# Kernel tuning notes

Hardware: AMD Instinct MI355X
Metric: run time of the kernel (lower is better)

Reference implementation:

```python
import jax, jax.numpy as jnp
import numpy as np

B, H, W, C = 1, 64, 512, 256
NH, HS, WS = 8, 4, 32
T = HS * WS            # tokens per window = 128
HD = C // NH           # head dim = 32
L = H * W
SCALE = HD ** -0.5
HID = 4 * C            # mlp hidden
EPS = 1e-5


def _ln(x, g, b):
    m = jnp.mean(x, axis=-1, keepdims=True)
    v = jnp.var(x, axis=-1, keepdims=True)
    return (x - m) * jax.lax.rsqrt(v + EPS) * g + b


def setup_inputs() -> dict:
    key = jax.random.key(0)
    ks = jax.random.split(key, 16)
    def rn(k, shape, s=0.02):
        return jax.random.normal(k, shape, jnp.float32) * s
    return {
        "x": jax.random.normal(ks[0], (B, L, C), jnp.float32),
        "pos": jax.random.normal(ks[1], (B, L, 2), jnp.float32),
        "norm1_g": jnp.ones((C,), jnp.float32), "norm1_b": jnp.zeros((C,), jnp.float32),
        "wq": rn(ks[2], (C, C)), "bq": jnp.zeros((C,), jnp.float32),
        "wk": rn(ks[3], (C, C)), "bk": jnp.zeros((C,), jnp.float32),
        "wv": rn(ks[4], (C, C)), "bv": jnp.zeros((C,), jnp.float32),
        "wo": rn(ks[5], (C, C)), "bo": jnp.zeros((C,), jnp.float32),
        "norm2_g": jnp.ones((C,), jnp.float32), "norm2_b": jnp.zeros((C,), jnp.float32),
        "w_fc1": rn(ks[6], (C, HID)), "b_fc1": jnp.zeros((HID,), jnp.float32),
        "w_fc2": rn(ks[7], (HID, C)), "b_fc2": jnp.zeros((C,), jnp.float32),
        # pos_embedding_cart: Conv1d(2->16,k1), BN1d(16) (inference), ReLU, Conv1d(16->NH,k1)
        "pw1": rn(ks[8], (16, 2), 0.1), "pb1": jnp.zeros((16,), jnp.float32),
        "bn_g": jnp.ones((16,), jnp.float32), "bn_b": jnp.zeros((16,), jnp.float32),
        "bn_m": jnp.zeros((16,), jnp.float32), "bn_v": jnp.ones((16,), jnp.float32),
        "pw2": rn(ks[9], (NH, 16), 0.1), "pb2": jnp.zeros((NH,), jnp.float32),
    }


def _to_windows(t):  # [B,L,C] -> [nW, T, C]
    t = t.reshape(B, H // HS, HS, W // WS, WS, C).transpose(0, 1, 3, 2, 4, 5)
    return t.reshape(-1, T, C)


def _to_heads(t):  # [B,L,C] -> [nW, NH, T, HD]
    return _to_windows(t).reshape(-1, T, NH, HD).transpose(0, 2, 1, 3)


def reference(x, pos, norm1_g, norm1_b, wq, bq, wk, bk, wv, bv, wo, bo,
              norm2_g, norm2_b, w_fc1, b_fc1, w_fc2, b_fc2,
              pw1, pb1, bn_g, bn_b, bn_m, bn_v, pw2, pb2):
    shortcut = x
    xn = _ln(x, norm1_g, norm1_b)

    # relative position bias per window via 1x1 conv net (BN in inference mode)
    posw = pos.reshape(B, H // HS, HS, W // WS, WS, 2).transpose(0, 1, 3, 5, 2, 4)
    posw = posw.reshape(-1, 2, T)                               # [nW, 2, T]
    rel = posw[:, :, :, None] - posw[:, :, None, :]             # [nW, 2, T, T]
    h = jnp.einsum('oc,nctu->notu', pw1, rel) + pb1[None, :, None, None]
    h = (h - bn_m[None, :, None, None]) * jax.lax.rsqrt(bn_v + EPS)[None, :, None, None]
    h = h * bn_g[None, :, None, None] + bn_b[None, :, None, None]
    h = jax.nn.relu(h)
    bias = jnp.einsum('oc,nctu->notu', pw2, h) + pb2[None, :, None, None]  # [nW, NH, T, T]

    q = _to_heads(xn @ wq + bq) * SCALE
    k = _to_heads(xn @ wk + bk)
    v = _to_heads(xn @ wv + bv)

    attn = jax.nn.softmax(jnp.einsum('nhtd,nhud->nhtu', q, k) + bias, axis=-1)
    o = jnp.einsum('nhtu,nhud->nhtd', attn, v)                  # [nW, NH, T, HD]
    o = o.transpose(0, 2, 1, 3).reshape(-1, T, C)               # [nW, T, C]
    o = o.reshape(B, H // HS, W // WS, HS, WS, C).transpose(0, 1, 3, 2, 4, 5)
    o = o.reshape(B, L, C) @ wo + bo

    x1 = shortcut + o
    mlp = jax.nn.gelu(_ln(x1, norm2_g, norm2_b) @ w_fc1 + b_fc1, approximate=False) @ w_fc2 + b_fc2
    return x1 + mlp
```

## Files before the change

### kernel.cpp

```cpp
#include <hip/hip_runtime.h>
#include <cstdint>

typedef unsigned short u16;
typedef __bf16 bf16x8 __attribute__((ext_vector_type(8)));
typedef float f32x4 __attribute__((ext_vector_type(4)));

#define LN_EPS 1e-5f
#define SCALE_Q 0.17677669529663689f

__device__ __forceinline__ u16 f2bf(float f) {
    union { float f; unsigned int i; } c; c.f = f;
    unsigned int r = c.i + 0x7FFFu + ((c.i >> 16) & 1u);
    return (u16)(r >> 16);
}
__device__ __forceinline__ unsigned pack2(float hi, float lo) {
    return __builtin_amdgcn_perm(__float_as_uint(hi), __float_as_uint(lo), 0x07060302u);
}
__device__ __forceinline__ void async16(const void* g, void* l) {
    __builtin_amdgcn_global_load_lds(
        (__attribute__((address_space(1))) unsigned int*)(unsigned long long)g,
        (__attribute__((address_space(3))) unsigned int*)l, 16, 0, 0);
}

__global__ void transpose_all(const float* __restrict__ wq, const float* __restrict__ wk,
                              const float* __restrict__ wv, const float* __restrict__ wo,
                              const float* __restrict__ f1, const float* __restrict__ f2,
                              u16* oq, u16* ok, u16* ov, u16* oo, u16* o1, u16* o2) {
    __shared__ float tile[32][33];
    const int b = blockIdx.x;
    const float* In; u16* Out; int R, C, bx, by;
    if (b < 256) {
        const int m = b >> 6, l = b & 63;
        In = m == 0 ? wq : (m == 1 ? wk : (m == 2 ? wv : wo));
        Out = m == 0 ? oq : (m == 1 ? ok : (m == 2 ? ov : oo));
        R = 256; C = 256; bx = (l & 7) * 32; by = (l >> 3) * 32;
    } else if (b < 512) {
        const int l = b - 256; In = f1; Out = o1; R = 256; C = 1024;
        bx = (l & 31) * 32; by = (l >> 5) * 32;
    } else {
        const int l = b - 512; In = f2; Out = o2; R = 1024; C = 256;
        bx = (l & 7) * 32; by = (l >> 3) * 32;
    }
    const int tx = threadIdx.x, ty = threadIdx.y;
    for (int i = 0; i < 32; i += 8)
        tile[ty + i][tx] = In[(size_t)(by + ty + i) * C + bx + tx];
    __syncthreads();
    for (int i = 0; i < 32; i += 8)
        Out[(size_t)(bx + ty + i) * R + by + tx] = f2bf(tile[tx][ty + i]);
}

__global__ __launch_bounds__(256) void ln_k(const float* __restrict__ X, const float* __restrict__ G,
                                            const float* __restrict__ Bt, u16* __restrict__ Y) {
    const int token = blockIdx.x * 4 + (threadIdx.x >> 6);
    const int ln = threadIdx.x & 63;
    const float4 rv = *(const float4*)(X + (size_t)token * 256 + ln * 4);
    float s = rv.x + rv.y + rv.z + rv.w;
    float q = rv.x * rv.x + rv.y * rv.y + rv.z * rv.z + rv.w * rv.w;
    #pragma unroll
    for (int m = 1; m < 64; m <<= 1) { s += __shfl_xor(s, m, 64); q += __shfl_xor(q, m, 64); }
    const float mean = s * (1.f / 256.f);
    const float var  = q * (1.f / 256.f) - mean * mean;
    const float rs   = rsqrtf(var + LN_EPS);
    const float4 gv = *(const float4*)(G + ln * 4);
    const float4 bv = *(const float4*)(Bt + ln * 4);
    ushort4 o;
    o.x = f2bf((rv.x - mean) * rs * gv.x + bv.x);
    o.y = f2bf((rv.y - mean) * rs * gv.y + bv.y);
    o.z = f2bf((rv.z - mean) * rs * gv.z + bv.z);
    o.w = f2bf((rv.w - mean) * rs * gv.w + bv.w);
    *(ushort4*)(Y + (size_t)token * 256 + ln * 4) = o;
}

__global__ __launch_bounds__(256, 2) void gemm_bt(
    const u16* __restrict__ X, const u16* __restrict__ Wt,
    const float* __restrict__ B1, const float* __restrict__ B2, const float* __restrict__ B3,
    const float* __restrict__ Res,
    u16* __restrict__ Ybf, float* __restrict__ Yf,
    int M, int N, int K, int mode) {
    __shared__ alignas(16) u16 sBuf[128 * 128];
    u16* sA = sBuf;
    u16* sB = sBuf + 128 * 64;
    const int tid = threadIdx.x, wv = tid >> 6, ln = tid & 63;
    const int quad = ln >> 4, l16 = ln & 15;
    const int m0 = blockIdx.y * 128, n0 = blockIdx.x * 128;
    const int mw = (wv >> 1) * 64, nw = (wv & 1) * 64;
    const int r8 = ln >> 3, c8 = ln & 7;
    const f32x4 z4 = {0.f, 0.f, 0.f, 0.f};
    f32x4 acc[4][4];
    #pragma unroll
    for (int i = 0; i < 4; i++)
        #pragma unroll
        for (int j = 0; j < 4; j++) acc[i][j] = z4;

    for (int k0 = 0; k0 < K; k0 += 64) {
        __syncthreads();
        #pragma unroll
        for (int i = 0; i < 4; i++) {
            const int row = wv * 32 + i * 8;
            async16(X  + (size_t)(m0 + row + r8) * K + k0 + c8 * 8, &sA[row * 64]);
            async16(Wt + (size_t)(n0 + row + r8) * K + k0 + c8 * 8, &sB[row * 64]);
        }
        __syncthreads();
        #pragma unroll
        for (int kk = 0; kk < 2; kk++) {
            bf16x8 af[4], bfr[4];
            #pragma unroll
            for (int i = 0; i < 4; i++) af[i]  = *(const bf16x8*)&sA[(mw + i * 16 + l16) * 64 + kk * 32 + quad * 8];
            #pragma unroll
            for (int j = 0; j < 4; j++) bfr[j] = *(const bf16x8*)&sB[(nw + j * 16 + l16) * 64 + kk * 32 + quad * 8];
            #pragma unroll
            for (int i = 0; i < 4; i++)
                #pragma unroll
                for (int j = 0; j < 4; j++)
                    acc[i][j] = __builtin_amdgcn_mfma_f32_16x16x32_bf16(af[i], bfr[j], acc[i][j], 0, 0, 0);
        }
    }
    const int seg = n0 >> 8;
    const float* bp = (mode == 4) ? (seg == 0 ? B1 : (seg == 1 ? B2 : B3)) : B1;
    const float sc = (mode == 4 && seg == 0) ? SCALE_Q : 1.f;
    if (mode == 4) {
        __syncthreads();
        #pragma unroll
        for (int j = 0; j < 4; j++) {
            const int col = nw + j * 16 + l16;
            const float bc = bp[(n0 + col) & 255];
            #pragma unroll
            for (int i = 0; i < 4; i++)
                #pragma unroll
                for (int r = 0; r < 4; r++)
                    sBuf[(mw + i * 16 + quad * 4 + r) * 128 + col] = f2bf((acc[i][j][r] + bc) * sc);
        }
        __syncthreads();
        #pragma unroll
        for (int it = 0; it < 8; it++) {
            const int idx = it * 256 + tid;
            const int row = idx >> 4, sg = idx & 15;
            *(uint4*)(Ybf + (size_t)(m0 + row) * N + n0 + sg * 8) = *(const uint4*)&sBuf[row * 128 + sg * 8];
        }
    } else {
        #pragma unroll
        for (int j = 0; j < 4; j++) {
            const int col = n0 + nw + j * 16 + l16;
            const float bc = bp[col];
            #pragma unroll
            for (int i = 0; i < 4; i++) {
                #pragma unroll
                for (int r = 0; r < 4; r++) {
                    const int row = m0 + mw + i * 16 + quad * 4 + r;
                    float v = acc[i][j][r] + bc;
                    if (mode == 2) v += Res[(size_t)row * N + col];
                    Yf[(size_t)row * N + col] = v;
                }
            }
        }
    }
}

__global__ __launch_bounds__(256) void bias_k(
    const float* __restrict__ pos, const float* __restrict__ pw1, const float* __restrict__ pb1,
    const float* __restrict__ bng, const float* __restrict__ bnb, const float* __restrict__ bnm,
    const float* __restrict__ bnv, const float* __restrict__ pw2, u16* __restrict__ Bg) {
    __shared__ float sTa[32 * 128], sTa2[32 * 128];
    __shared__ u16 sW[16 * 32];
    __shared__ alignas(16) u16 sOut[4][8 * 128];
    const int n = blockIdx.x, wh = n >> 4, ww = n & 15;
    const int tid = threadIdx.x, wv = tid >> 6, ln = tid & 63;
    const int quad = ln >> 4, l16 = ln & 15;
    for (int r = 0; r < 16; r++) {
        const int e = tid + r * 256, o = e >> 7, t = e & 127;
        float ta = 0.f, ta2 = 0.f;
        if (o < 16) {
            const int l = (wh * 4 + (t >> 5)) * 512 + ww * 32 + (t & 31);
            const float sv = rsqrtf(bnv[o] + LN_EPS) * bng[o];
            ta = sv * (pw1[o * 2] * pos[l * 2] + pw1[o * 2 + 1] * pos[l * 2 + 1]);
            ta2 = ta + (pb1[o] - bnm[o]) * sv + bnb[o];
        }
        sTa[o * 128 + t] = ta; sTa2[o * 128 + t] = ta2;
    }
    for (int r = 0; r < 2; r++) {
        const int e = tid + r * 256, h = e >> 5, o = e & 31;
        sW[e] = (h < 8 && o < 16) ? f2bf(pw2[h * 16 + o]) : (u16)0;
    }
    __syncthreads();
    const bf16x8 af = *(const bf16x8*)&sW[l16 * 32 + quad * 8];
    float uo[8][8];
    #pragma unroll
    for (int c = 0; c < 8; c++)
        #pragma unroll
        for (int j = 0; j < 8; j++)
            uo[c][j] = sTa[(quad * 8 + j) * 128 + c * 16 + l16];
    const f32x4 z4 = {0.f, 0.f, 0.f, 0.f};
    u16* outb = Bg + (size_t)n * 131072;
    for (int tl = 0; tl < 32; tl++) {
        const int t = wv * 32 + tl;
        float t2[8];
        #pragma unroll
        for (int j = 0; j < 8; j++) t2[j] = sTa2[(quad * 8 + j) * 128 + t];
        #pragma unroll
        for (int c = 0; c < 8; c++) {
            float rl[8];
            #pragma unroll
            for (int j = 0; j < 8; j++) rl[j] = fmaxf(t2[j] - uo[c][j], 0.f);
            union { unsigned u[4]; bf16x8 v; } bb;
            #pragma unroll
            for (int p = 0; p < 4; p++) bb.u[p] = pack2(rl[2 * p + 1], rl[2 * p]);
            const f32x4 cc = __builtin_amdgcn_mfma_f32_16x16x32_bf16(af, bb.v, z4, 0, 0, 0);
            if (quad < 2) {
                #pragma unroll
                for (int r = 0; r < 4; r++)
                    sOut[wv][(quad * 4 + r) * 128 + c * 16 + l16] =
                        (u16)(__float_as_uint(cc[r]) >> 16);
            }
        }
        #pragma unroll
        for (int it = 0; it < 2; it++) {
            const int idx = it * 64 + ln;
            const int h = idx >> 4, u8 = idx & 15;
            *(uint4*)(outb + (size_t)h * 16384 + t * 128 + u8 * 8) = *(const uint4*)&sOut[wv][idx * 8];
        }
    }
}

__global__ __launch_bounds__(256, 2) void attn_k(
    const u16* __restrict__ Qkv, const u16* __restrict__ Bg, u16* __restrict__ Ob) {
    constexpr int SPS = 136;
    __shared__ alignas(16) u16 sQ[128 * 32];
    __shared__ alignas(16) u16 sK[128 * 32];
    __shared__ alignas(16) u16 sVt[32 * 128];
    __shared__ alignas(16) u16 sPB[128 * SPS];

    const int n = blockIdx.x, h = blockIdx.y;
    const int tid = threadIdx.x, wv = tid >> 6, ln = tid & 63;
    const int quad = ln >> 4, l16 = ln & 15;
    const int wh = n >> 4, ww = n & 15;

    {
        const int tb = wv * 16 + (ln >> 2);
        const int d8 = ln & 3;
        #pragma unroll
        for (int i = 0; i < 2; i++) {
            const int tt = tb + i * 64;
            const int l = (wh * 4 + (tt >> 5)) * 512 + ww * 32 + (tt & 31);
            const size_t g = (size_t)l * 768 + h * 32 + d8 * 8;
            async16(Qkv + g, &sQ[(wv * 16 + i * 64) * 32]);
            async16(Qkv + g + 256, &sK[(wv * 16 + i * 64) * 32]);
        }
        const u16* bsrc = Bg + (size_t)(n * 8 + h) * 16384;
        #pragma unroll
        for (int rr = 0; rr < 8; rr++)
            async16(bsrc + rr * 2048 + wv * 512 + ln * 8, &sPB[rr * 2048 + wv * 512]);
        #pragma unroll
        for (int i = 0; i < 2; i++) {
            const int tt = tb + i * 64;
            const int l = (wh * 4 + (tt >> 5)) * 512 + ww * 32 + (tt & 31);
            const uint4 raw = *(const uint4*)(Qkv + (size_t)l * 768 + 512 + h * 32 + d8 * 8);
            const u16* e = (const u16*)&raw;
            #pragma unroll
            for (int j = 0; j < 8; j++) sVt[(d8 * 8 + j) * 128 + tt] = e[j];
        }
    }
    __syncthreads();

    const f32x4 z4 = {0.f, 0.f, 0.f, 0.f};
    f32x4 acc[2][8];
    {
        bf16x8 qf[2], kf[8];
        #pragma unroll
        for (int i = 0; i < 2; i++) qf[i] = *(const bf16x8*)&sQ[(wv * 32 + i * 16 + l16) * 32 + quad * 8];
        #pragma unroll
        for (int j = 0; j < 8; j++) kf[j] = *(const bf16x8*)&sK[(j * 16 + l16) * 32 + quad * 8];
        #pragma unroll
        for (int i = 0; i < 2; i++)
            #pragma unroll
            for (int j = 0; j < 8; j++)
                acc[i][j] = __builtin_amdgcn_mfma_f32_16x16x32_bf16(qf[i], kf[j], z4, 0, 0, 0);
    }
    #pragma unroll
    for (int i = 0; i < 2; i++)
        #pragma unroll
        for (int j = 0; j < 8; j++)
            #pragma unroll
            for (int r = 0; r < 4; r++) {
                const int t = wv * 32 + i * 16 + quad * 4 + r;
                const unsigned bu = sPB[t * 128 + j * 16 + l16];
                acc[i][j][r] += __uint_as_float(bu << 16);
            }
    float rinv[2][4];
    #pragma unroll
    for (int i = 0; i < 2; i++) {
        #pragma unroll
        for (int r = 0; r < 4; r++) {
            float mx = acc[i][0][r];
            #pragma unroll
            for (int j = 1; j < 8; j++) mx = fmaxf(mx, acc[i][j][r]);
            #pragma unroll
            for (int m = 1; m < 16; m <<= 1) mx = fmaxf(mx, __shfl_xor(mx, m, 64));
            float sm = 0.f;
            #pragma unroll
            for (int j = 0; j < 8; j++) {
                const float p = __expf(acc[i][j][r] - mx);
                acc[i][j][r] = p;
                sm += p;
            }
            #pragma unroll
            for (int m = 1; m < 16; m <<= 1) sm += __shfl_xor(sm, m, 64);
            rinv[i][r] = 1.f / sm;
        }
    }
    __syncthreads();
    #pragma unroll
    for (int i = 0; i < 2; i++)
        #pragma unroll
        for (int j = 0; j < 8; j++)
            #pragma unroll
            for (int r = 0; r < 4; r++) {
                const int t = wv * 32 + i * 16 + quad * 4 + r;
                sPB[t * SPS + j * 16 + l16] = (u16)(__float_as_uint(acc[i][j][r]) >> 16);
            }
    __syncthreads();
    f32x4 oacc[2][2];
    #pragma unroll
    for (int i = 0; i < 2; i++)
        #pragma unroll
        for (int jd = 0; jd < 2; jd++) oacc[i][jd] = z4;
    #pragma unroll
    for (int ku = 0; ku < 4; ku++) {
        bf16x8 pf[2], vf[2];
        #pragma unroll
        for (int i = 0; i < 2; i++) pf[i] = *(const bf16x8*)&sPB[(wv * 32 + i * 16 + l16) * SPS + ku * 32 + quad * 8];
        #pragma unroll
        for (int jd = 0; jd < 2; jd++) vf[jd] = *(const bf16x8*)&sVt[(jd * 16 + l16) * 128 + ku * 32 + quad * 8];
        #pragma unroll
        for (int i = 0; i < 2; i++)
            #pragma unroll
            for (int jd = 0; jd < 2; jd++)
                oacc[i][jd] = __builtin_amdgcn_mfma_f32_16x16x32_bf16(pf[i], vf[jd], oacc[i][jd], 0, 0, 0);
    }
    #pragma unroll
    for (int i = 0; i < 2; i++)
        #pragma unroll
        for (int jd = 0; jd < 2; jd++)
            #pragma unroll
            for (int r = 0; r < 4; r++) {
                const int t = wv * 32 + i * 16 + quad * 4 + r;
                const int d = jd * 16 + l16;
                const int l = (wh * 4 + (t >> 5)) * 512 + ww * 32 + (t & 31);
                Ob[(size_t)l * 256 + h * 32 + d] = f2bf(oacc[i][jd][r] * rinv[i][r]);
            }
}

__global__ __launch_bounds__(256, 2) void mlp_fused(
    const u16* __restrict__ Xn, const u16* __restrict__ fc1T, const u16* __restrict__ fc2T,
    const float* __restrict__ b1, const float* __restrict__ b2, float* __restrict__ Out) {
    __shared__ alignas(16) u16 sA[64 * 256];
    __shared__ alignas(16) u16 sW[128 * 128];
    __shared__ alignas(16) u16 sH[64 * 128];
    const int tid = threadIdx.x, wv = tid >> 6, ln = tid & 63;
    const int quad = ln >> 4, l16 = ln & 15;
    const int m0 = blockIdx.x * 64;
    const int mw = (wv >> 1) * 32;
    const int nw1 = (wv & 1) * 64;
    const int nw2 = (wv & 1) * 128;

    #pragma unroll
    for (int rr = 0; rr < 8; rr++) {
        const int row2 = rr * 8 + wv * 2;
        const int row = row2 + (ln >> 5);
        const int kb = (ln & 31) ^ (row & 7);
        async16(Xn + (size_t)(m0 + row) * 256 + kb * 8, &sA[row2 * 256]);
    }

    const f32x4 z4 = {0.f, 0.f, 0.f, 0.f};
    f32x4 acc2[2][8];
    #pragma unroll
    for (int i = 0; i < 2; i++)
        #pragma unroll
        for (int j = 0; j < 8; j++) acc2[i][j] = z4;

    for (int c = 0; c < 8; c++) {
        f32x4 acc1[2][4];
        #pragma unroll
        for (int i = 0; i < 2; i++)
            #pragma unroll
            for (int j = 0; j < 4; j++) acc1[i][j] = z4;
        #pragma unroll
        for (int kc0 = 0; kc0 < 2; kc0++) {
            __syncthreads();
            #pragma unroll
            for (int rr = 0; rr < 8; rr++) {
                const int r4 = wv * 32 + rr * 4;
                const int row = r4 + (ln >> 4);
                const int kb = (ln & 15) ^ (row & 15);
                async16(fc1T + (size_t)(c * 128 + row) * 256 + kc0 * 128 + kb * 8, &sW[r4 * 128]);
            }
            __syncthreads();
            #pragma unroll
            for (int kk = 0; kk < 4; kk++) {
                bf16x8 af[2], bfr[4];
                #pragma unroll
                for (int i = 0; i < 2; i++) {
                    const int ra = mw + i * 16 + l16;
                    const int b = kc0 * 16 + kk * 4 + quad;
                    af[i] = *(const bf16x8*)&sA[ra * 256 + ((b ^ (ra & 7)) * 8)];
                }
                #pragma unroll
                for (int j = 0; j < 4; j++) {
                    const int rb = nw1 + j * 16 + l16;
                    const int b = kk * 4 + quad;
                    bfr[j] = *(const bf16x8*)&sW[rb * 128 + ((b ^ (rb & 15)) * 8)];
                }
                #pragma unroll
                for (int i = 0; i < 2; i++)
                    #pragma unroll
                    for (int j = 0; j < 4; j++)
                        acc1[i][j] = __builtin_amdgcn_mfma_f32_16x16x32_bf16(af[i], bfr[j], acc1[i][j], 0, 0, 0);
            }
        }
        #pragma unroll
        for (int j = 0; j < 4; j++) {
            const float bc = b1[c * 128 + nw1 + j * 16 + l16];
            const int col = nw1 + j * 16 + l16;
            const int blk = col >> 3, off = col & 7;
            #pragma unroll
            for (int i = 0; i < 2; i++)
                #pragma unroll
                for (int r = 0; r < 4; r++) {
                    float v = acc1[i][j][r] + bc;
                    const float p = v * v;
                    const float qq = fmaf(p, -0.07135481283f, -1.5957691216f);
                    v = v / (1.f + __expf(v * qq));
                    const int row = mw + i * 16 + quad * 4 + r;
                    sH[row * 128 + ((blk ^ (row & 15)) * 8) + off] = f2bf(v);
                }
        }
        #pragma unroll
        for (int kc0 = 0; kc0 < 2; kc0++) {
            __syncthreads();
            #pragma unroll
            for (int rr = 0; rr < 8; rr++) {
                const int r8 = wv * 64 + rr * 8;
                const int row = r8 + (ln >> 3);
                const int kb = (ln & 7) ^ (row & 7);
                async16(fc2T + (size_t)row * 1024 + c * 128 + kc0 * 64 + kb * 8, &sW[r8 * 64]);
            }
            __syncthreads();
            #pragma unroll
            for (int kk = 0; kk < 2; kk++) {
                bf16x8 pf[2], bfr[8];
                #pragma unroll
                for (int i = 0; i < 2; i++) {
                    const int rp = mw + i * 16 + l16;
                    const int b = kc0 * 8 + kk * 4 + quad;
                    pf[i] = *(const bf16x8*)&sH[rp * 128 + ((b ^ (rp & 15)) * 8)];
                }
                #pragma unroll
                for (int j = 0; j < 8; j++) {
                    const int rb = nw2 + j * 16 + l16;
                    const int b = kk * 4 + quad;
                    bfr[j] = *(const bf16x8*)&sW[rb * 64 + ((b ^ (rb & 7)) * 8)];
                }
                #pragma unroll
                for (int i = 0; i < 2; i++)
                    #pragma unroll
                    for (int j = 0; j < 8; j++)
                        acc2[i][j] = __builtin_amdgcn_mfma_f32_16x16x32_bf16(pf[i], bfr[j], acc2[i][j], 0, 0, 0);
            }
        }
    }
    #pragma unroll
    for (int j = 0; j < 8; j++) {
        const int col = nw2 + j * 16 + l16;
        const float bc = b2[col];
        #pragma unroll
        for (int i = 0; i < 2; i++)
            #pragma unroll
            for (int r = 0; r < 4; r++) {
                const size_t idx = (size_t)(m0 + mw + i * 16 + quad * 4 + r) * 256 + col;
                Out[idx] = acc2[i][j][r] + bc + Out[idx];
            }
    }
}

extern "C" void kernel_launch(void* const* d_in, const int* in_sizes, int n_in,
                              void* d_out, int out_size, void* d_ws, size_t ws_size,
                              hipStream_t stream) {
    const float* x    = (const float*)d_in[0];
    const float* pos  = (const float*)d_in[1];
    const float* n1g  = (const float*)d_in[2];
    const float* n1b  = (const float*)d_in[3];
    const float* wq   = (const float*)d_in[4];
    const float* bq   = (const float*)d_in[5];
    const float* wk   = (const float*)d_in[6];
    const float* bk   = (const float*)d_in[7];
    const float* wvw  = (const float*)d_in[8];
    const float* bv   = (const float*)d_in[9];
    const float* wo   = (const float*)d_in[10];
    const float* bo   = (const float*)d_in[11];
    const float* n2g  = (const float*)d_in[12];
    const float* n2b  = (const float*)d_in[13];
    const float* wfc1 = (const float*)d_in[14];
    const float* bfc1 = (const float*)d_in[15];
    const float* wfc2 = (const float*)d_in[16];
    const float* bfc2 = (const float*)d_in[17];
    const float* pw1  = (const float*)d_in[18];
    const float* pb1  = (const float*)d_in[19];
    const float* bng  = (const float*)d_in[20];
    const float* bnb  = (const float*)d_in[21];
    const float* bnm  = (const float*)d_in[22];
    const float* bnv  = (const float*)d_in[23];
    const float* pw2  = (const float*)d_in[24];
    float* out = (float*)d_out;
    u16* ws  = (u16*)d_ws;

    const size_t SZ = (size_t)32768 * 256;
    u16* s0   = ws;
    u16* qkv  = ws + SZ;
    u16* wqT  = ws + 4 * SZ;
    u16* wkT  = wqT + 65536;
    u16* wvT  = wkT + 65536;
    u16* woT  = wvT + 65536;
    u16* fc1T = woT + 65536;
    u16* fc2T = fc1T + 262144;
    u16* biasg = fc2T + 262144;

    transpose_all<<<768, dim3(32, 8), 0, stream>>>(wq, wk, wvw, wo, wfc1, wfc2,
                                                   wqT, wkT, wvT, woT, fc1T, fc2T);
    ln_k<<<8192, 256, 0, stream>>>(x, n1g, n1b, s0);
    gemm_bt<<<dim3(6, 256), 256, 0, stream>>>(s0, wqT, bq, bk, bv, nullptr, qkv, nullptr,
                                              32768, 768, 256, 4);
    bias_k<<<256, 256, 0, stream>>>(pos, pw1, pb1, bng, bnb, bnm, bnv, pw2, biasg);
    attn_k<<<dim3(256, 8), 256, 0, stream>>>(qkv, biasg, s0);
    gemm_bt<<<dim3(2, 256), 256, 0, stream>>>(s0, woT, bo, nullptr, nullptr, x, nullptr, out,
                                              32768, 256, 256, 2);
    ln_k<<<8192, 256, 0, stream>>>(out, n2g, n2b, s0);
    mlp_fused<<<512, 256, 0, stream>>>(s0, fc1T, fc2T, bfc1, bfc2, out);
}
```

Before: 322.4 us.

## Swizzle LDS layouts in gemm/attn and double-buffer fused MLP weight staging

Applies XOR swizzles to the LDS tiles in the generic GEMM (A and B) and in the attention kernel (Q, K and transposed V), so that MFMA fragment reads and V scatter writes avoid bank conflicts. In the fused MLP kernel, the single 128x128 weight buffer is split into two 64x128 ping-pong buffers with smaller k-chunks. The next fc1/fc2 chunk, and the first fc1 chunk of the following column block, now prefetch while the current chunk is computed. This removes one barrier per stage and hides global load latency, in exchange for more chunks and more complex index arithmetic.

```diff
diff --git a/kernel.cpp b/kernel.cpp
--- a/kernel.cpp
+++ b/kernel.cpp
@@ -84,7 +84,8 @@
     const int quad = ln >> 4, l16 = ln & 15;
     const int m0 = blockIdx.y * 128, n0 = blockIdx.x * 128;
     const int mw = (wv >> 1) * 64, nw = (wv & 1) * 64;
-    const int r8 = ln >> 3, c8 = ln & 7;
+    const int r8 = ln >> 3;
+    const int kbs = (ln & 7) ^ (r8 & 7);
     const f32x4 z4 = {0.f, 0.f, 0.f, 0.f};
     f32x4 acc[4][4];
     #pragma unroll
@@ -97,17 +98,25 @@
         #pragma unroll
         for (int i = 0; i < 4; i++) {
             const int row = wv * 32 + i * 8;
-            async16(X  + (size_t)(m0 + row + r8) * K + k0 + c8 * 8, &sA[row * 64]);
-            async16(Wt + (size_t)(n0 + row + r8) * K + k0 + c8 * 8, &sB[row * 64]);
+            async16(X  + (size_t)(m0 + row + r8) * K + k0 + kbs * 8, &sA[row * 64]);
+            async16(Wt + (size_t)(n0 + row + r8) * K + k0 + kbs * 8, &sB[row * 64]);
         }
         __syncthreads();
         #pragma unroll
         for (int kk = 0; kk < 2; kk++) {
             bf16x8 af[4], bfr[4];
             #pragma unroll
-            for (int i = 0; i < 4; i++) af[i]  = *(const bf16x8*)&sA[(mw + i * 16 + l16) * 64 + kk * 32 + quad * 8];
-            #pragma unroll
-            for (int j = 0; j < 4; j++) bfr[j] = *(const bf16x8*)&sB[(nw + j * 16 + l16) * 64 + kk * 32 + quad * 8];
+            for (int i = 0; i < 4; i++) {
+                const int ra = mw + i * 16 + l16;
+                const int b = kk * 4 + quad;
+                af[i] = *(const bf16x8*)&sA[ra * 64 + ((b ^ (ra & 7)) * 8)];
+            }
+            #pragma unroll
+            for (int j = 0; j < 4; j++) {
+                const int rb = nw + j * 16 + l16;
+                const int b = kk * 4 + quad;
+                bfr[j] = *(const bf16x8*)&sB[rb * 64 + ((b ^ (rb & 7)) * 8)];
+            }
             #pragma unroll
             for (int i = 0; i < 4; i++)
                 #pragma unroll
@@ -235,13 +244,14 @@
     const int wh = n >> 4, ww = n & 15;
 
     {
-        const int tb = wv * 16 + (ln >> 2);
-        const int d8 = ln & 3;
+        const int rw = ln >> 2;
+        const int tb = wv * 16 + rw;
+        const int kbq = (ln & 3) ^ (rw & 3);
         #pragma unroll
         for (int i = 0; i < 2; i++) {
             const int tt = tb + i * 64;
             const int l = (wh * 4 + (tt >> 5)) * 512 + ww * 32 + (tt & 31);
-            const size_t g = (size_t)l * 768 + h * 32 + d8 * 8;
+            const size_t g = (size_t)l * 768 + h * 32 + kbq * 8;
             async16(Qkv + g, &sQ[(wv * 16 + i * 64) * 32]);
             async16(Qkv + g + 256, &sK[(wv * 16 + i * 64) * 32]);
         }
@@ -249,6 +259,7 @@
         #pragma unroll
         for (int rr = 0; rr < 8; rr++)
             async16(bsrc + rr * 2048 + wv * 512 + ln * 8, &sPB[rr * 2048 + wv * 512]);
+        const int d8 = ln & 3;
         #pragma unroll
         for (int i = 0; i < 2; i++) {
             const int tt = tb + i * 64;
@@ -256,7 +267,10 @@
             const uint4 raw = *(const uint4*)(Qkv + (size_t)l * 768 + 512 + h * 32 + d8 * 8);
             const u16* e = (const u16*)&raw;
             #pragma unroll
-            for (int j = 0; j < 8; j++) sVt[(d8 * 8 + j) * 128 + tt] = e[j];
+            for (int j = 0; j < 8; j++) {
+                const int row = d8 * 8 + j;
+                sVt[row * 128 + (((tt >> 3) ^ (row & 15)) * 8) + (tt & 7)] = e[j];
+            }
         }
     }
     __syncthreads();
@@ -266,9 +280,15 @@
     {
         bf16x8 qf[2], kf[8];
         #pragma unroll
-        for (int i = 0; i < 2; i++) qf[i] = *(const bf16x8*)&sQ[(wv * 32 + i * 16 + l16) * 32 + quad * 8];
-        #pragma unroll
-        for (int j = 0; j < 8; j++) kf[j] = *(const bf16x8*)&sK[(j * 16 + l16) * 32 + quad * 8];
+        for (int i = 0; i < 2; i++) {
+            const int t = wv * 32 + i * 16 + l16;
+            qf[i] = *(const bf16x8*)&sQ[t * 32 + ((quad ^ (t & 3)) * 8)];
+        }
+        #pragma unroll
+        for (int j = 0; j < 8; j++) {
+            const int t = j * 16 + l16;
+            kf[j] = *(const bf16x8*)&sK[t * 32 + ((quad ^ (t & 3)) * 8)];
+        }
         #pragma unroll
         for (int i = 0; i < 2; i++)
             #pragma unroll
@@ -329,7 +349,11 @@
         #pragma unroll
         for (int i = 0; i < 2; i++) pf[i] = *(const bf16x8*)&sPB[(wv * 32 + i * 16 + l16) * SPS + ku * 32 + quad * 8];
         #pragma unroll
-        for (int jd = 0; jd < 2; jd++) vf[jd] = *(const bf16x8*)&sVt[(jd * 16 + l16) * 128 + ku * 32 + quad * 8];
+        for (int jd = 0; jd < 2; jd++) {
+            const int rv = jd * 16 + l16;
+            const int b = ku * 4 + quad;
+            vf[jd] = *(const bf16x8*)&sVt[rv * 128 + ((b ^ (rv & 15)) * 8)];
+        }
         #pragma unroll
         for (int i = 0; i < 2; i++)
             #pragma unroll
@@ -353,7 +377,8 @@
     const u16* __restrict__ Xn, const u16* __restrict__ fc1T, const u16* __restrict__ fc2T,
     const float* __restrict__ b1, const float* __restrict__ b2, float* __restrict__ Out) {
     __shared__ alignas(16) u16 sA[64 * 256];
-    __shared__ alignas(16) u16 sW[128 * 128];
+    __shared__ alignas(16) u16 sW0[64 * 128];
+    __shared__ alignas(16) u16 sW1[64 * 128];
     __shared__ alignas(16) u16 sH[64 * 128];
     const int tid = threadIdx.x, wv = tid >> 6, ln = tid & 63;
     const int quad = ln >> 4, l16 = ln & 15;
@@ -362,6 +387,25 @@
     const int nw1 = (wv & 1) * 64;
     const int nw2 = (wv & 1) * 128;
 
+    auto stage_f1 = [&](int c, int kc, u16* buf) {
+        #pragma unroll
+        for (int rr = 0; rr < 4; rr++) {
+            const int r0 = (rr * 4 + wv) * 8;
+            const int row = r0 + (ln >> 3);
+            const int kb = (ln & 7) ^ (row & 7);
+            async16(fc1T + (size_t)(c * 128 + row) * 256 + kc * 64 + kb * 8, &buf[r0 * 64]);
+        }
+    };
+    auto stage_f2 = [&](int c, int kc, u16* buf) {
+        #pragma unroll
+        for (int rr = 0; rr < 4; rr++) {
+            const int r0 = (rr * 4 + wv) * 16;
+            const int row = r0 + (ln >> 2);
+            const int kb = (ln & 3) ^ (row & 3);
+            async16(fc2T + (size_t)row * 1024 + c * 128 + kc * 32 + kb * 8, &buf[r0 * 32]);
+        }
+    };
+
     #pragma unroll
     for (int rr = 0; rr < 8; rr++) {
         const int row2 = rr * 8 + wv * 2;
@@ -369,6 +413,7 @@
         const int kb = (ln & 31) ^ (row & 7);
         async16(Xn + (size_t)(m0 + row) * 256 + kb * 8, &sA[row2 * 256]);
     }
+    stage_f1(0, 0, sW0);
 
     const f32x4 z4 = {0.f, 0.f, 0.f, 0.f};
     f32x4 acc2[2][8];
@@ -377,6 +422,7 @@
         #pragma unroll
         for (int j = 0; j < 8; j++) acc2[i][j] = z4;
 
+    __syncthreads();
     for (int c = 0; c < 8; c++) {
         f32x4 acc1[2][4];
         #pragma unroll
@@ -384,30 +430,24 @@
             #pragma unroll
             for (int j = 0; j < 4; j++) acc1[i][j] = z4;
         #pragma unroll
-        for (int kc0 = 0; kc0 < 2; kc0++) {
-            __syncthreads();
-            #pragma unroll
-            for (int rr = 0; rr < 8; rr++) {
-                const int r4 = wv * 32 + rr * 4;
-                const int row = r4 + (ln >> 4);
-                const int kb = (ln & 15) ^ (row & 15);
-                async16(fc1T + (size_t)(c * 128 + row) * 256 + kc0 * 128 + kb * 8, &sW[r4 * 128]);
-            }
-            __syncthreads();
-            #pragma unroll
-            for (int kk = 0; kk < 4; kk++) {
+        for (int kc = 0; kc < 4; kc++) {
+            u16* cur = (kc & 1) ? sW1 : sW0;
+            u16* nxt = (kc & 1) ? sW0 : sW1;
+            if (kc < 3) stage_f1(c, kc + 1, nxt);
+            #pragma unroll
+            for (int kk = 0; kk < 2; kk++) {
                 bf16x8 af[2], bfr[4];
                 #pragma unroll
                 for (int i = 0; i < 2; i++) {
                     const int ra = mw + i * 16 + l16;
-                    const int b = kc0 * 16 + kk * 4 + quad;
+                    const int b = kc * 8 + kk * 4 + quad;
                     af[i] = *(const bf16x8*)&sA[ra * 256 + ((b ^ (ra & 7)) * 8)];
                 }
                 #pragma unroll
                 for (int j = 0; j < 4; j++) {
                     const int rb = nw1 + j * 16 + l16;
                     const int b = kk * 4 + quad;
-                    bfr[j] = *(const bf16x8*)&sW[rb * 128 + ((b ^ (rb & 15)) * 8)];
+                    bfr[j] = *(const bf16x8*)&cur[rb * 64 + ((b ^ (rb & 7)) * 8)];
                 }
                 #pragma unroll
                 for (int i = 0; i < 2; i++)
@@ -415,7 +455,9 @@
                     for (int j = 0; j < 4; j++)
                         acc1[i][j] = __builtin_amdgcn_mfma_f32_16x16x32_bf16(af[i], bfr[j], acc1[i][j], 0, 0, 0);
             }
-        }
+            __syncthreads();
+        }
+        stage_f2(c, 0, sW0);
         #pragma unroll
         for (int j = 0; j < 4; j++) {
             const float bc = b1[c * 128 + nw1 + j * 16 + l16];
@@ -433,38 +475,31 @@
                     sH[row * 128 + ((blk ^ (row & 15)) * 8) + off] = f2bf(v);
                 }
         }
-        #pragma unroll
-        for (int kc0 = 0; kc0 < 2; kc0++) {
+        __syncthreads();
+        #pragma unroll
+        for (int kc = 0; kc < 4; kc++) {
+            u16* cur = (kc & 1) ? sW1 : sW0;
+            u16* nxt = (kc & 1) ? sW0 : sW1;
+            if (kc < 3) stage_f2(c, kc + 1, nxt);
+            else if (c < 7) stage_f1(c + 1, 0, nxt);
+            bf16x8 pf[2], bfr[8];
+            #pragma unroll
+            for (int i = 0; i < 2; i++) {
+                const int rp = mw + i * 16 + l16;
+                const int b = kc * 4 + quad;
+                pf[i] = *(const bf16x8*)&sH[rp * 128 + ((b ^ (rp & 15)) * 8)];
+            }
+            #pragma unroll
+            for (int j = 0; j < 8; j++) {
+                const int rb = nw2 + j * 16 + l16;
+                bfr[j] = *(const bf16x8*)&cur[rb * 32 + ((quad ^ (rb & 3)) * 8)];
+            }
+            #pragma unroll
+            for (int i = 0; i < 2; i++)
+                #pragma unroll
+                for (int j = 0; j < 8; j++)
+                    acc2[i][j] = __builtin_amdgcn_mfma_f32_16x16x32_bf16(pf[i], bfr[j], acc2[i][j], 0, 0, 0);
             __syncthreads();
-            #pragma unroll
-            for (int rr = 0; rr < 8; rr++) {
-                const int r8 = wv * 64 + rr * 8;
-                const int row = r8 + (ln >> 3);
-                const int kb = (ln & 7) ^ (row & 7);
-                async16(fc2T + (size_t)row * 1024 + c * 128 + kc0 * 64 + kb * 8, &sW[r8 * 64]);
-            }
-            __syncthreads();
-            #pragma unroll
-            for (int kk = 0; kk < 2; kk++) {
-                bf16x8 pf[2], bfr[8];
-                #pragma unroll
-                for (int i = 0; i < 2; i++) {
-                    const int rp = mw + i * 16 + l16;
-                    const int b = kc0 * 8 + kk * 4 + quad;
-                    pf[i] = *(const bf16x8*)&sH[rp * 128 + ((b ^ (rp & 15)) * 8)];
-                }
-                #pragma unroll
-                for (int j = 0; j < 8; j++) {
-                    const int rb = nw2 + j * 16 + l16;
-                    const int b = kk * 4 + quad;
-                    bfr[j] = *(const bf16x8*)&sW[rb * 64 + ((b ^ (rb & 7)) * 8)];
-                }
-                #pragma unroll
-                for (int i = 0; i < 2; i++)
-                    #pragma unroll
-                    for (int j = 0; j < 8; j++)
-                        acc2[i][j] = __builtin_amdgcn_mfma_f32_16x16x32_bf16(pf[i], bfr[j], acc2[i][j], 0, 0, 0);
-            }
         }
     }
     #pragma unroll
```

After: 320.4 us. About the same (-0.6%).
